# Performance work log

Measured on AMD Instinct MI355X. Metric: run time of the kernel, lower is better.

## Reference

```python
import jax, jax.numpy as jnp
import numpy as np
from jax import lax

VOCAB, D, H, S, W, OUT = 100000, 300, 50, 64, 32, 5


def setup_inputs() -> dict:
    key = jax.random.key(0)
    ks = jax.random.split(key, 32)
    g = lambda i, shape, scale=0.05: (jax.random.normal(ks[i], shape, dtype=jnp.float32) * scale)
    inp = {
        'doc': jax.random.randint(ks[0], (S, W), 0, VOCAB),
        'emb': g(1, (VOCAB, D)),
        'wl_w': g(2, (H, D)), 'wl_b': g(3, (H,)),
        'c1_w': g(4, (H, H, 1)), 'c1_b': g(5, (H,)),
        'c2_w': g(6, (H, H, 2)), 'c2_b': g(7, (H,)),
        'c3_w': g(8, (H, H, 3)), 'c3_b': g(9, (H,)),
        'f_i_w': g(10, (H, 2 * H)), 'f_i_b': g(11, (H,)),
        'f_f_w': g(12, (H, 2 * H)), 'f_f_b': g(13, (H,)),
        'f_g_w': g(14, (H, 2 * H)), 'f_g_b': g(15, (H,)),
        'b_i_w': g(16, (H, 2 * H)), 'b_i_b': g(17, (H,)),
        'b_f_w': g(18, (H, 2 * H)), 'b_f_b': g(19, (H,)),
        'b_g_w': g(20, (H, 2 * H)), 'b_g_b': g(21, (H,)),
        'out_w': g(22, (OUT, 2 * H)), 'out_b': g(23, (OUT,)),
    }
    return inp


def _conv_rep(x, w, b):
    # x: [S, H, W]; w: [O, I, k] torch-style conv1d weight
    y = lax.conv_general_dilated(x, w, window_strides=(1,), padding='VALID',
                                 dimension_numbers=('NCH', 'OIH', 'NCH'))
    y = y + b[None, :, None]
    return jnp.tanh(y.mean(axis=2))  # [S, H]  (avg-pool over full length then tanh)


def _gnn_scan(reps, Wi, bi, Wf, bf, Wg, bg):
    # reps: [S, H]; sequential gated cell
    def step(h, r):
        comp = jnp.concatenate([r, h])  # [2H]
        i = jax.nn.sigmoid(comp @ Wi.T + bi)
        f = jax.nn.sigmoid(comp @ Wf.T + bf)
        g = jnp.tanh(comp @ Wg.T + bg)
        h_t = jnp.tanh(i * g + f * h)
        return h_t, h_t
    _, hs = lax.scan(step, jnp.zeros(reps.shape[1], dtype=reps.dtype), reps)
    return hs  # [S, H]


def reference(doc, emb, wl_w, wl_b, c1_w, c1_b, c2_w, c2_b, c3_w, c3_b,
              f_i_w, f_i_b, f_f_w, f_f_b, f_g_w, f_g_b,
              b_i_w, b_i_b, b_f_w, b_f_b, b_g_w, b_g_b, out_w, out_b):
    x = emb[doc]                                  # [S, W, D]
    p = jnp.einsum('swd,hd->swh', x, wl_w) + wl_b # word_linear, [S, W, H]
    xc = p.transpose(0, 2, 1)                     # [S, H, W]
    # sentence_convolution: mean over the 3 kernel-size branches
    rep = (_conv_rep(xc, c1_w, c1_b) + _conv_rep(xc, c2_w, c2_b) + _conv_rep(xc, c3_w, c3_b)) / 3.0
    h_f = _gnn_scan(rep, f_i_w, f_i_b, f_f_w, f_f_b, f_g_w, f_g_b)         # forward pass
    h_b = _gnn_scan(rep[::-1], b_i_w, b_i_b, b_f_w, b_f_b, b_g_w, b_g_b)[::-1]  # backward pass, realigned
    gnn_out = jnp.concatenate([h_f, h_b], axis=1).mean(axis=0)             # [2H]
    logits = gnn_out @ out_w.T + out_b
    return jax.nn.softmax(logits)
```

## Files before the change

kernel.cpp:

```cpp
#include <hip/hip_runtime.h>
#include <hip/hip_fp16.h>


__device__ __forceinline__ float rl(float v, int j) {
    return __uint_as_float((unsigned)__builtin_amdgcn_readlane(__float_as_uint(v), j));
}
__device__ __forceinline__ float sigm(float x) { return 1.f / (1.f + __expf(-x)); }
__device__ __forceinline__ float tanh_fast(float x) {
    return 1.f - 2.f / (__expf(2.f * x) + 1.f);
}

__global__ __launch_bounds__(320, 1) void rep_kernel(
    const int* __restrict__ doc, const float* __restrict__ emb,
    const float* __restrict__ wl_w, const float* __restrict__ wl_b,
    const float* __restrict__ c1w, const float* __restrict__ c1b,
    const float* __restrict__ c2w, const float* __restrict__ c2b,
    const float* __restrict__ c3w, const float* __restrict__ c3b,
    const float* __restrict__ fiw, const float* __restrict__ fib,
    const float* __restrict__ ffw, const float* __restrict__ ffb,
    const float* __restrict__ fgw, const float* __restrict__ fgb,
    const float* __restrict__ biw, const float* __restrict__ bib,
    const float* __restrict__ bfw, const float* __restrict__ bfb,
    const float* __restrict__ bgw, const float* __restrict__ bgb,
    float* __restrict__ preW)
{
    __shared__ int docs[32];
    __shared__ float xL[32][300];
    __shared__ float sv[5][300];
    __shared__ float P[5][50];
    __shared__ float m[6][50];
    __shared__ float part[6][50];
    __shared__ float r[50];

    const int s = blockIdx.x, tid = threadIdx.x;
    if (tid < 32) docs[tid] = doc[s * 32 + tid];
    __syncthreads();

    {
        const float4* ef4 = (const float4*)emb;
        float4* xf4 = (float4*)&xL[0][0];
        for (int idx = tid; idx < 2400; idx += 320) {
            const int rr = idx / 75, c = idx - rr * 75;
            xf4[idx] = ef4[docs[rr] * 75 + c];
        }
    }
    __syncthreads();

    if (tid < 300) {
        float a = 0.f;
#pragma unroll
        for (int w = 0; w < 32; ++w) a += xL[w][tid];
        sv[0][tid] = a;
        sv[1][tid] = xL[0][tid];
        sv[2][tid] = xL[1][tid];
        sv[3][tid] = xL[30][tid];
        sv[4][tid] = xL[31][tid];
    }
    __syncthreads();

    if (tid < 250) {
        const int i = tid / 5, v = tid - (tid / 5) * 5;
        const float2* wrow = (const float2*)(wl_w + i * 300);
        float a0 = 0.f, a1 = 0.f;
#pragma unroll 5
        for (int d2 = 0; d2 < 150; ++d2) {
            float2 wv = wrow[d2];
            a0 = fmaf(wv.x, sv[v][2 * d2],     a0);
            a1 = fmaf(wv.y, sv[v][2 * d2 + 1], a1);
        }
        P[v][i] = a0 + a1;
    }
    __syncthreads();

    if (tid < 50) {
        const int i = tid;
        const float b  = wl_b[i];
        const float QA = P[0][i], Q0 = P[1][i], Q1 = P[2][i],
                    Q30 = P[3][i], Q31 = P[4][i];
        m[0][i] = QA * (1.f / 32.f) + b;
        m[1][i] = (QA - Q31) * (1.f / 31.f) + b;
        m[2][i] = (QA - Q0)  * (1.f / 31.f) + b;
        m[3][i] = (QA - Q30 - Q31) * (1.f / 30.f) + b;
        m[4][i] = (QA - Q0  - Q31) * (1.f / 30.f) + b;
        m[5][i] = (QA - Q0  - Q1 ) * (1.f / 30.f) + b;
    }
    __syncthreads();

    if (tid < 300) {
        const int q = tid / 50, o = tid - q * 50;
        const float* base = (q == 0) ? c1w : (q < 3) ? c2w : c3w;
        const int str = (q == 0) ? 1 : (q < 3) ? 2 : 3;
        const int off = (q == 0) ? 0 : (q < 3) ? (q - 1) : (q - 3);
        float acc = (q == 0) ? c1b[o] : (q == 1) ? c2b[o] : (q == 3) ? c3b[o] : 0.f;
        const float* mp = m[q];
#pragma unroll 5
        for (int i = 0; i < 50; ++i)
            acc = fmaf(base[(o * 50 + i) * str + off], mp[i], acc);
        part[q][o] = acc;
    }
    __syncthreads();
    if (tid < 50) {
        const float y1 = tanh_fast(part[0][tid]);
        const float y2 = tanh_fast(part[1][tid] + part[2][tid]);
        const float y3 = tanh_fast(part[3][tid] + part[4][tid] + part[5][tid]);
        r[tid] = (y1 + y2 + y3) * (1.f / 3.f);
    }
    __syncthreads();

    if (tid < 300) {
        const int g = tid / 50, o = tid - g * 50;
        const float* Wg = (g == 0) ? fiw : (g == 1) ? ffw : (g == 2) ? fgw
                        : (g == 3) ? biw : (g == 4) ? bfw : bgw;
        const float* Bg = (g == 0) ? fib : (g == 1) ? ffb : (g == 2) ? fgb
                        : (g == 3) ? bib : (g == 4) ? bfb : bgb;
        const int sp = (g < 3) ? s : (63 - s);
        const float2* wrow = (const float2*)(Wg + o * 100);
        float acc = Bg[o];
#pragma unroll
        for (int j2 = 0; j2 < 25; ++j2) {
            float2 wv = wrow[j2];
            acc = fmaf(wv.x, r[2 * j2], fmaf(wv.y, r[2 * j2 + 1], acc));
        }
        preW[g * 3200 + sp * 50 + o] = acc;
    }
}

__global__ __launch_bounds__(128, 1) void scan_kernel(
    const float* __restrict__ preW,
    const float* __restrict__ fiw, const float* __restrict__ ffw,
    const float* __restrict__ fgw, const float* __restrict__ biw,
    const float* __restrict__ bfw, const float* __restrict__ bgw,
    const float* __restrict__ out_w, const float* __restrict__ out_b,
    float* __restrict__ outp)
{
    __shared__ float pre[6][64][50];
    __shared__ float mh[2][52];
    __shared__ float lg[5];

    const int tid = threadIdx.x;
    const int d = tid >> 6, lane = tid & 63;
    const int oc = (lane < 50) ? lane : 0;

    {
        const float2* src = (const float2*)preW;
        float2* dst = (float2*)&pre[0][0][0];
#pragma unroll
        for (int k = 0; k < 75; ++k) dst[tid + 128 * k] = src[tid + 128 * k];
    }

    const float* Wi = d ? biw : fiw;
    const float* Wf = d ? bfw : ffw;
    const float* Wg = d ? bgw : fgw;
    __half2 hwi[25], hwf[25], hwg[25];
    {
        const float2* ri = (const float2*)(Wi + oc * 100 + 50);
        const float2* rf = (const float2*)(Wf + oc * 100 + 50);
        const float2* rg = (const float2*)(Wg + oc * 100 + 50);
#pragma unroll
        for (int k = 0; k < 25; ++k) {
            float2 a = ri[k], b = rf[k], c = rg[k];
            hwi[k] = __floats2half2_rn(a.x, a.y);
            hwf[k] = __floats2half2_rn(b.x, b.y);
            hwg[k] = __floats2half2_rn(c.x, c.y);
        }
    }
    __syncthreads();

    const int g0 = d * 3;
    float h = 0.f, hsum = 0.f;
    float nai = pre[g0 + 0][0][oc];
    float naf = pre[g0 + 1][0][oc];
    float nag = pre[g0 + 2][0][oc];
#pragma unroll 1
    for (int s2 = 0; s2 < 64; ++s2) {
        float ai = nai, af = naf, ag = nag;
        if (s2 < 63) {
            nai = pre[g0 + 0][s2 + 1][oc];
            naf = pre[g0 + 1][s2 + 1][oc];
            nag = pre[g0 + 2][s2 + 1][oc];
        }
#pragma unroll
        for (int k = 0; k < 25; ++k) {
            const float h0 = rl(h, 2 * k);
            const float h1 = rl(h, 2 * k + 1);
            ai = fmaf(__low2float(hwi[k]), h0, fmaf(__high2float(hwi[k]), h1, ai));
            af = fmaf(__low2float(hwf[k]), h0, fmaf(__high2float(hwf[k]), h1, af));
            ag = fmaf(__low2float(hwg[k]), h0, fmaf(__high2float(hwg[k]), h1, ag));
        }
        h = tanh_fast(fmaf(sigm(ai), tanh_fast(ag), sigm(af) * h));
        hsum += h;
    }
    if (lane < 50) mh[d][lane] = hsum * (1.f / 64.f);
    __syncthreads();

    if (tid < 5) {
        const float2* wrow = (const float2*)(out_w + tid * 100);
        float acc = out_b[tid];
#pragma unroll
        for (int j2 = 0; j2 < 25; ++j2) {
            float2 wv2 = wrow[j2];
            acc = fmaf(wv2.x, mh[0][2 * j2], fmaf(wv2.y, mh[0][2 * j2 + 1], acc));
        }
#pragma unroll
        for (int j2 = 0; j2 < 25; ++j2) {
            float2 wv2 = wrow[25 + j2];
            acc = fmaf(wv2.x, mh[1][2 * j2], fmaf(wv2.y, mh[1][2 * j2 + 1], acc));
        }
        lg[tid] = acc;
    }
    __syncthreads();
    if (tid == 0) {
        float mx = lg[0];
#pragma unroll
        for (int k = 1; k < 5; ++k) mx = fmaxf(mx, lg[k]);
        float e[5], se = 0.f;
#pragma unroll
        for (int k = 0; k < 5; ++k) { e[k] = __expf(lg[k] - mx); se += e[k]; }
        const float inv = 1.f / se;
#pragma unroll
        for (int k = 0; k < 5; ++k) outp[k] = e[k] * inv;
    }
}

extern "C" void kernel_launch(void* const* d_in, const int* in_sizes, int n_in,
                              void* d_out, int out_size, void* d_ws, size_t ws_size,
                              hipStream_t stream)
{
    (void)in_sizes; (void)n_in; (void)out_size; (void)ws_size;
    const int*   doc  = (const int*)  d_in[0];
    const float* emb  = (const float*)d_in[1];
    const float* wl_w = (const float*)d_in[2];
    const float* wl_b = (const float*)d_in[3];
    const float* c1w  = (const float*)d_in[4];
    const float* c1b  = (const float*)d_in[5];
    const float* c2w  = (const float*)d_in[6];
    const float* c2b  = (const float*)d_in[7];
    const float* c3w  = (const float*)d_in[8];
    const float* c3b  = (const float*)d_in[9];
    const float* fiw  = (const float*)d_in[10];
    const float* fib  = (const float*)d_in[11];
    const float* ffw  = (const float*)d_in[12];
    const float* ffb  = (const float*)d_in[13];
    const float* fgw  = (const float*)d_in[14];
    const float* fgb  = (const float*)d_in[15];
    const float* biw  = (const float*)d_in[16];
    const float* bib  = (const float*)d_in[17];
    const float* bfw  = (const float*)d_in[18];
    const float* bfb  = (const float*)d_in[19];
    const float* bgw  = (const float*)d_in[20];
    const float* bgb  = (const float*)d_in[21];
    const float* ow   = (const float*)d_in[22];
    const float* ob   = (const float*)d_in[23];

    float* preW = (float*)d_ws;

    rep_kernel<<<64, 320, 0, stream>>>(doc, emb, wl_w, wl_b,
                                       c1w, c1b, c2w, c2b, c3w, c3b,
                                       fiw, fib, ffw, ffb, fgw, fgb,
                                       biw, bib, bfw, bfb, bgw, bgb, preW);
    scan_kernel<<<1, 128, 0, stream>>>(preW, fiw, ffw, fgw, biw, bfw, bgw,
                                       ow, ob, (float*)d_out);
}
```

Before: 258.8 us.

## Stage word-linear weights in LDS and split dot products across more threads

The rep kernel grows from 320 to 512 threads. It copies the full 50x300 word_linear weight matrix into shared memory in parallel with the embedding gather. The word-projection dot products are split in half across twice as many threads and the two halves are summed afterward. The conv reductions use two accumulators to shorten the dependency chain. This adds about 60KB of LDS traffic per block and a larger block size, in exchange for shorter serial FMA chains in the rep phase.

```diff
diff --git a/kernel.cpp b/kernel.cpp
--- a/kernel.cpp
+++ b/kernel.cpp
@@ -10,7 +10,7 @@
     return 1.f - 2.f / (__expf(2.f * x) + 1.f);
 }
 
-__global__ __launch_bounds__(320, 1) void rep_kernel(
+__global__ __launch_bounds__(512, 1) void rep_kernel(
     const int* __restrict__ doc, const float* __restrict__ emb,
     const float* __restrict__ wl_w, const float* __restrict__ wl_b,
     const float* __restrict__ c1w, const float* __restrict__ c1b,
@@ -24,24 +24,36 @@
     const float* __restrict__ bgw, const float* __restrict__ bgb,
     float* __restrict__ preW)
 {
-    __shared__ int docs[32];
+    __shared__ float wlw[15000];
     __shared__ float xL[32][300];
     __shared__ float sv[5][300];
-    __shared__ float P[5][50];
-    __shared__ float m[6][50];
-    __shared__ float part[6][50];
-    __shared__ float r[50];
+    __shared__ float Ph[2][5][52];
+    __shared__ float m[6][52];
+    __shared__ float part[6][52];
+    __shared__ float r[52];
+    __shared__ int docs[32];
 
     const int s = blockIdx.x, tid = threadIdx.x;
     if (tid < 32) docs[tid] = doc[s * 32 + tid];
     __syncthreads();
 
     {
+        const float4* wsrc = (const float4*)wl_w;
+        float4* wdst = (float4*)wlw;
+#pragma unroll
+        for (int k = 0; k < 8; ++k) {
+            const int idx = tid + 512 * k;
+            if (idx < 3750) wdst[idx] = wsrc[idx];
+        }
         const float4* ef4 = (const float4*)emb;
         float4* xf4 = (float4*)&xL[0][0];
-        for (int idx = tid; idx < 2400; idx += 320) {
-            const int rr = idx / 75, c = idx - rr * 75;
-            xf4[idx] = ef4[docs[rr] * 75 + c];
+#pragma unroll
+        for (int k = 0; k < 5; ++k) {
+            const int idx = tid + 512 * k;
+            if (idx < 2400) {
+                const int rr = idx / 75, c = idx - rr * 75;
+                xf4[idx] = ef4[docs[rr] * 75 + c];
+            }
         }
     }
     __syncthreads();
@@ -58,25 +70,29 @@
     }
     __syncthreads();
 
-    if (tid < 250) {
-        const int i = tid / 5, v = tid - (tid / 5) * 5;
-        const float2* wrow = (const float2*)(wl_w + i * 300);
+    if (tid < 500) {
+        const int i = tid / 10, rem = tid - i * 10, v = rem >> 1, hf = rem & 1;
+        const float2* w2 = (const float2*)(wlw + i * 300 + hf * 150);
+        const float2* x2 = (const float2*)(sv[v] + hf * 150);
         float a0 = 0.f, a1 = 0.f;
-#pragma unroll 5
-        for (int d2 = 0; d2 < 150; ++d2) {
-            float2 wv = wrow[d2];
-            a0 = fmaf(wv.x, sv[v][2 * d2],     a0);
-            a1 = fmaf(wv.y, sv[v][2 * d2 + 1], a1);
-        }
-        P[v][i] = a0 + a1;
+#pragma unroll
+        for (int k = 0; k < 75; ++k) {
+            const float2 w = w2[k], x = x2[k];
+            a0 = fmaf(w.x, x.x, a0);
+            a1 = fmaf(w.y, x.y, a1);
+        }
+        Ph[hf][v][i] = a0 + a1;
     }
     __syncthreads();
 
     if (tid < 50) {
         const int i = tid;
-        const float b  = wl_b[i];
-        const float QA = P[0][i], Q0 = P[1][i], Q1 = P[2][i],
-                    Q30 = P[3][i], Q31 = P[4][i];
+        const float b   = wl_b[i];
+        const float QA  = Ph[0][0][i] + Ph[1][0][i];
+        const float Q0  = Ph[0][1][i] + Ph[1][1][i];
+        const float Q1  = Ph[0][2][i] + Ph[1][2][i];
+        const float Q30 = Ph[0][3][i] + Ph[1][3][i];
+        const float Q31 = Ph[0][4][i] + Ph[1][4][i];
         m[0][i] = QA * (1.f / 32.f) + b;
         m[1][i] = (QA - Q31) * (1.f / 31.f) + b;
         m[2][i] = (QA - Q0)  * (1.f / 31.f) + b;
@@ -91,12 +107,15 @@
         const float* base = (q == 0) ? c1w : (q < 3) ? c2w : c3w;
         const int str = (q == 0) ? 1 : (q < 3) ? 2 : 3;
         const int off = (q == 0) ? 0 : (q < 3) ? (q - 1) : (q - 3);
-        float acc = (q == 0) ? c1b[o] : (q == 1) ? c2b[o] : (q == 3) ? c3b[o] : 0.f;
+        float a0 = (q == 0) ? c1b[o] : (q == 1) ? c2b[o] : (q == 3) ? c3b[o] : 0.f;
+        float a1 = 0.f;
         const float* mp = m[q];
-#pragma unroll 5
-        for (int i = 0; i < 50; ++i)
-            acc = fmaf(base[(o * 50 + i) * str + off], mp[i], acc);
-        part[q][o] = acc;
+#pragma unroll
+        for (int i = 0; i < 50; i += 2) {
+            a0 = fmaf(base[(o * 50 + i)     * str + off], mp[i],     a0);
+            a1 = fmaf(base[(o * 50 + i + 1) * str + off], mp[i + 1], a1);
+        }
+        part[q][o] = a0 + a1;
     }
     __syncthreads();
     if (tid < 50) {
@@ -118,7 +137,7 @@
         float acc = Bg[o];
 #pragma unroll
         for (int j2 = 0; j2 < 25; ++j2) {
-            float2 wv = wrow[j2];
+            const float2 wv = wrow[j2];
             acc = fmaf(wv.x, r[2 * j2], fmaf(wv.y, r[2 * j2 + 1], acc));
         }
         preW[g * 3200 + sp * 50 + o] = acc;
@@ -254,7 +273,7 @@
 
     float* preW = (float*)d_ws;
 
-    rep_kernel<<<64, 320, 0, stream>>>(doc, emb, wl_w, wl_b,
+    rep_kernel<<<64, 512, 0, stream>>>(doc, emb, wl_w, wl_b,
                                        c1w, c1b, c2w, c2b, c3w, c3b,
                                        fiw, fib, ffw, ffb, fgw, fgb,
                                        biw, bib, bfw, bfb, bgw, bgb, preW);
```

New measurement: 244.1 us. -5.7%, faster.
